# Optimization experiments

Measured on AMD Instinct MI355X. Metric: run time of the kernel, lower is better.

The kernel has to match this reference:

```python
import jax, jax.numpy as jnp
from jax import lax
import numpy as np

# --- config (torchvision Mask R-CNN RPN / RoIAlign defaults) ---
IMG = 800.0        # image size (square)
STRIDE = 4.0       # FPN level stride -> feature 200x200
K_PRE = 2000       # pre-NMS top-k proposals
K_POST = 512       # post-NMS proposals kept
IOU_THR = 0.7      # RPN NMS IoU threshold
OUT = 7            # RoIAlign output size
SR = 2             # RoIAlign sampling ratio
SCALE = 1.0 / STRIDE
BBOX_XFORM_CLIP = 4.135166556742356  # log(1000/16)


def setup_inputs() -> dict:
    key = jax.random.key(0)
    k1, k2, k3 = jax.random.split(key, 3)
    C, H, W = 256, 200, 200
    feature = jax.random.normal(k1, (C, H, W), jnp.float32)
    # anchor grid: 3 sizes per location, stride 4 (proper geometric anchors)
    sizes = np.array([32.0, 64.0, 128.0], np.float32)
    ys, xs = np.meshgrid(np.arange(H, dtype=np.float32) * STRIDE,
                         np.arange(W, dtype=np.float32) * STRIDE, indexing='ij')
    ctr = np.stack([xs, ys], axis=-1).reshape(-1, 1, 2)            # [HW,1,2] (x,y)
    half = np.stack([sizes / 2, sizes / 2], axis=-1)[None]          # [1,3,2]
    anchors = np.concatenate([ctr - half + 0 * half, ctr + half], axis=-1)
    anchors = np.broadcast_to(np.concatenate([ctr - half, ctr + half], -1),
                              (H * W, 3, 4)).reshape(-1, 4).astype(np.float32)
    N = anchors.shape[0]  # 120000
    objectness = jax.random.normal(k2, (N,), jnp.float32)
    deltas = jax.random.normal(k3, (N, 4), jnp.float32) * 0.1
    return {"feature": feature, "objectness": objectness,
            "deltas": deltas, "anchors": jnp.asarray(anchors)}


def decode_boxes(deltas, anchors):
    w = anchors[:, 2] - anchors[:, 0]
    h = anchors[:, 3] - anchors[:, 1]
    cx = anchors[:, 0] + 0.5 * w
    cy = anchors[:, 1] + 0.5 * h
    dx, dy = deltas[:, 0], deltas[:, 1]
    dw = jnp.minimum(deltas[:, 2], BBOX_XFORM_CLIP)
    dh = jnp.minimum(deltas[:, 3], BBOX_XFORM_CLIP)
    pcx = dx * w + cx
    pcy = dy * h + cy
    pw = jnp.exp(dw) * w
    ph = jnp.exp(dh) * h
    boxes = jnp.stack([pcx - 0.5 * pw, pcy - 0.5 * ph,
                       pcx + 0.5 * pw, pcy + 0.5 * ph], axis=-1)
    return jnp.clip(boxes, 0.0, IMG)


def pairwise_iou(b):  # b: [K,4]
    area = (b[:, 2] - b[:, 0]) * (b[:, 3] - b[:, 1])
    lt = jnp.maximum(b[:, None, :2], b[None, :, :2])
    rb = jnp.minimum(b[:, None, 2:], b[None, :, 2:])
    wh = jnp.maximum(rb - lt, 0.0)
    inter = wh[..., 0] * wh[..., 1]
    return inter / (area[:, None] + area[None, :] - inter + 1e-6)


def nms_suppress(boxes_sorted, iou_thr):
    # boxes sorted by descending score; returns keep mask [K]
    K = boxes_sorted.shape[0]
    iou = pairwise_iou(boxes_sorted)
    js = jnp.arange(K)
    def body(i, supp):
        row = (iou[i] > iou_thr) & (js > i)
        return jnp.where(supp[i], supp, supp | row)
    supp = lax.fori_loop(0, K, body, jnp.zeros((K,), bool))
    return ~supp


def roi_align(feature, boxes):
    # feature: [C,H,W]; boxes: [M,4] in image coords; aligned=False variant
    C, H, W = feature.shape
    P = OUT * SR
    def one(box):
        x1, y1, x2, y2 = box[0] * SCALE, box[1] * SCALE, box[2] * SCALE, box[3] * SCALE
        rw = jnp.maximum(x2 - x1, 1.0)
        rh = jnp.maximum(y2 - y1, 1.0)
        idx = jnp.arange(P, dtype=feature.dtype) + 0.5
        ys = y1 + idx * (rh / P)   # [P]
        xs = x1 + idx * (rw / P)
        yy, xx = jnp.meshgrid(ys, xs, indexing='ij')     # [P,P]
        y = jnp.clip(yy, 0.0, H - 1.0)
        x = jnp.clip(xx, 0.0, W - 1.0)
        y0 = jnp.floor(y).astype(jnp.int32)
        x0 = jnp.floor(x).astype(jnp.int32)
        y1i = jnp.minimum(y0 + 1, H - 1)
        x1i = jnp.minimum(x0 + 1, W - 1)
        ly = y - y0.astype(feature.dtype)
        lx = x - x0.astype(feature.dtype)
        v00 = feature[:, y0, x0]    # [C,P,P]
        v01 = feature[:, y0, x1i]
        v10 = feature[:, y1i, x0]
        v11 = feature[:, y1i, x1i]
        val = (v00 * (1 - ly) * (1 - lx) + v01 * (1 - ly) * lx
               + v10 * ly * (1 - lx) + v11 * ly * lx)  # [C,P,P]
        return val.reshape(C, OUT, SR, OUT, SR).mean(axis=(2, 4))  # [C,7,7]
    return jax.vmap(one)(boxes)


def reference(feature, objectness, deltas, anchors):
    boxes = decode_boxes(deltas, anchors)                    # [N,4]
    scores, idx = lax.top_k(objectness, K_PRE)               # pre-NMS top-k
    cand = boxes[idx]                                        # [K_PRE,4] sorted
    keep = nms_suppress(cand, IOU_THR)                       # [K_PRE] bool
    masked = jnp.where(keep, scores, -jnp.inf)
    _, fidx = lax.top_k(masked, K_POST)                      # post-NMS top-k
    final_boxes = cand[fidx]                                 # [K_POST,4]
    valid = keep[fidx].astype(feature.dtype)                 # [K_POST]
    roi = roi_align(feature, final_boxes)                    # [K_POST,256,7,7]
    return roi * valid[:, None, None, None]
```

## Files before the change

kernel.cpp:

```cpp
#include <hip/hip_runtime.h>
#include <cstdint>
#include <cstddef>

#define N_ANCH   120000
#define K_PRE    2000
#define K_POST   512
#define CAP      4096
#define NWORD    32
#define HBINS    4096
#define IOU_THR  0.7f
#define IMGF     800.0f
#define CLIPV    4.135166556742356f
#define FH       200
#define FW       200
#define FC       256
#define SCALE    0.25f

#define TROWS    96
#define NTILE    21
#define CH       8

#define CG       16
#define TPE      4

typedef unsigned long long u64;
typedef float f2u __attribute__((ext_vector_type(2), aligned(4)));

struct Ws {
    uint32_t T;
    uint32_t cnt;
    int32_t  nk;
    uint32_t pad;
    u64      combo[CAP];
    float4   cand[K_PRE];
    int      rows[K_POST];
    u64      mask[(size_t)K_PRE * NWORD];
};

__device__ inline uint32_t fkey(float f) {
    uint32_t u = __float_as_uint(f);
    return (u & 0x80000000u) ? ~u : (u | 0x80000000u);
}

__global__ __launch_bounds__(1024) void zero_k(Ws* __restrict__ ws) {
    uint32_t* h = (uint32_t*)ws->mask;
    for (int i = threadIdx.x; i < HBINS; i += 1024) h[i] = 0u;
    if (threadIdx.x == 0) { ws->cnt = 0u; ws->nk = 0; ws->T = 0u; }
}

__global__ __launch_bounds__(256) void hist_k(const float* __restrict__ obj,
                                              uint32_t* __restrict__ hist) {
    __shared__ uint32_t h[HBINS];
    for (int i = threadIdx.x; i < HBINS; i += 256) h[i] = 0u;
    __syncthreads();
    const float4* o4 = (const float4*)obj;
    for (int i = blockIdx.x * 256 + threadIdx.x; i < N_ANCH / 4; i += gridDim.x * 256) {
        float4 v = o4[i];
        atomicAdd(&h[fkey(v.x) >> 20], 1u);
        atomicAdd(&h[fkey(v.y) >> 20], 1u);
        atomicAdd(&h[fkey(v.z) >> 20], 1u);
        atomicAdd(&h[fkey(v.w) >> 20], 1u);
    }
    __syncthreads();
    for (int i = threadIdx.x; i < HBINS; i += 256)
        if (h[i]) atomicAdd(&hist[i], h[i]);
}

__global__ __launch_bounds__(256) void gather_k(const float* __restrict__ obj,
                                                const uint32_t* __restrict__ hist,
                                                Ws* __restrict__ ws) {
    __shared__ uint32_t wsum[4];
    __shared__ uint32_t sT;
    const int tid = threadIdx.x;
    const int lane = tid & 63, wave = tid >> 6;
    uint32_t c[16]; uint32_t s = 0;
#pragma unroll
    for (int k = 0; k < 16; ++k) { c[k] = hist[HBINS - 1 - (16 * tid + k)]; s += c[k]; }
    uint32_t incl = s;
    for (int off = 1; off < 64; off <<= 1) {
        uint32_t t = __shfl_up(incl, off);
        if (lane >= off) incl += t;
    }
    if (lane == 63) wsum[wave] = incl;
    __syncthreads();
    uint32_t wpre = 0;
    for (int w2 = 0; w2 < wave; ++w2) wpre += wsum[w2];
    uint32_t before = wpre + incl - s;
#pragma unroll
    for (int k = 0; k < 16; ++k) {
        uint32_t after = before + c[k];
        if (before < K_PRE && after >= K_PRE)
            sT = (uint32_t)(HBINS - 1 - (16 * tid + k)) << 20;
        before = after;
    }
    __syncthreads();
    const uint32_t T = sT;
    int i = blockIdx.x * 256 + tid;
    if (i >= N_ANCH / 4) return;
    float4 v = ((const float4*)obj)[i];
    float vals[4] = {v.x, v.y, v.z, v.w};
#pragma unroll
    for (int k = 0; k < 4; ++k) {
        uint32_t u = fkey(vals[k]);
        if (u >= T) {
            uint32_t pos = atomicAdd(&ws->cnt, 1u);
            if (pos < CAP)
                ws->combo[pos] = ((u64)(~u) << 32) | (uint32_t)(4 * i + k);
        }
    }
}

__global__ __launch_bounds__(256) void rank_decode_k(const float* __restrict__ deltas,
                                                     const float* __restrict__ anchors,
                                                     Ws* __restrict__ ws) {
    __shared__ u64 sc[CAP];
    const int tid = threadIdx.x;
    int M = (int)ws->cnt;
    if (M > CAP) M = CAP;
    const int ebase = blockIdx.x * (256 / TPE);
    if (ebase >= M) return;
    for (int e = tid; e < M; e += 256) sc[e] = ws->combo[e];
    __syncthreads();
    const int gid = ebase + tid / TPE;
    const int sub = tid & (TPE - 1);
    if (gid >= M) return;
    const u64 mine = sc[gid];
    int cnt = 0;
    int j = sub;
    for (; j + 3 * TPE < M; j += 4 * TPE) {
        u64 a = sc[j], b = sc[j + TPE], c = sc[j + 2 * TPE], d = sc[j + 3 * TPE];
        cnt += (int)(a < mine) + (int)(b < mine) + (int)(c < mine) + (int)(d < mine);
    }
    for (; j < M; j += TPE) cnt += (int)(sc[j] < mine);
    cnt += __shfl_xor(cnt, 1);
    cnt += __shfl_xor(cnt, 2);
    if (sub == 0 && cnt < K_PRE) {
        const uint32_t idx = (uint32_t)(mine & 0xFFFFFFFFull);
        float a0 = anchors[idx * 4 + 0], a1 = anchors[idx * 4 + 1];
        float a2 = anchors[idx * 4 + 2], a3 = anchors[idx * 4 + 3];
        float d0 = deltas[idx * 4 + 0],  d1 = deltas[idx * 4 + 1];
        float d2 = fminf(deltas[idx * 4 + 2], CLIPV);
        float d3 = fminf(deltas[idx * 4 + 3], CLIPV);
        float w = a2 - a0, h = a3 - a1;
        float cx = a0 + 0.5f * w, cy = a1 + 0.5f * h;
        float pcx = d0 * w + cx, pcy = d1 * h + cy;
        float pw = expf(d2) * w, ph = expf(d3) * h;
        float x1 = fminf(fmaxf(pcx - 0.5f * pw, 0.0f), IMGF);
        float y1 = fminf(fmaxf(pcy - 0.5f * ph, 0.0f), IMGF);
        float x2 = fminf(fmaxf(pcx + 0.5f * pw, 0.0f), IMGF);
        float y2 = fminf(fmaxf(pcy + 0.5f * ph, 0.0f), IMGF);
        ws->cand[cnt] = make_float4(x1, y1, x2, y2);
    }
}

__global__ __launch_bounds__(256) void nms_mask_k(Ws* __restrict__ ws) {
    const int i = blockIdx.x;
    const int lane = threadIdx.x & 63;
    const int wave = threadIdx.x >> 6;
    const float4 bi = ws->cand[i];
    const float ai = (bi.z - bi.x) * (bi.w - bi.y);
    for (int wd = wave; wd < NWORD; wd += 4) {
        int j = wd * 64 + lane;
        bool bit = false;
        if (j < K_PRE && j > i) {
            float4 bj = ws->cand[j];
            float aj = (bj.z - bj.x) * (bj.w - bj.y);
            float xx1 = fmaxf(bi.x, bj.x);
            float yy1 = fmaxf(bi.y, bj.y);
            float xx2 = fminf(bi.z, bj.z);
            float yy2 = fminf(bi.w, bj.w);
            float ww = fmaxf(xx2 - xx1, 0.0f);
            float hh = fmaxf(yy2 - yy1, 0.0f);
            float inter = ww * hh;
            float iou = inter / (ai + aj - inter + 1e-6f);
            bit = iou > IOU_THR;
        }
        u64 bal = __ballot(bit);
        if (lane == 0) ws->mask[(size_t)i * NWORD + wd] = bal;
    }
}

__global__ __launch_bounds__(512) void scan_roi_k(const float* __restrict__ feat,
                                                  Ws* __restrict__ ws,
                                                  float* __restrict__ out) {
    __shared__ __align__(16) u64 sbuf[2][TROWS * NWORD];
    __shared__ int s_stop;
    __shared__ int sRow;
    const int tid = threadIdx.x;
    const int lane = tid & 63;
    const int wave = tid >> 6;

    if (blockIdx.x == 0) {
        const int lmod = lane & 31;
        const u64* __restrict__ mask = ws->mask;
        {
            const ulonglong2* src = (const ulonglong2*)mask;
            ulonglong2* dst = (ulonglong2*)sbuf[0];
            for (int e = tid; e < TROWS * NWORD / 2; e += 512) dst[e] = src[e];
        }
        if (tid == 0) s_stop = 0;
        __syncthreads();

        u64 supp = 0ull;
        int pubtot = 0;
        const u64 valid = (lane < NWORD - 1) ? ~0ull
                        : (lane == NWORD - 1 ? ((1ull << (K_PRE - (NWORD - 1) * 64)) - 1ull)
                                             : 0ull);
        for (int t = 0; t < NTILE; ++t) {
            const int base = t * TROWS;
            const int nb = min(TROWS, K_PRE - base);
            if (wave == 0) {
                const u64* sm = sbuf[t & 1];
                u64 A[CH], B[CH];
#pragma unroll
                for (int b = 0; b < CH; ++b) A[b] = sm[b * NWORD + lmod];
                for (int s = 0; s < nb; s += 2 * CH) {
                    const bool hasB = (s + CH) < nb;
                    if (hasB) {
#pragma unroll
                        for (int b = 0; b < CH; ++b) B[b] = sm[(s + CH + b) * NWORD + lmod];
                    }
                    {
                        const int w = (base + s) >> 6;
                        const int bofs = (base + s) & 63;
                        u64 keptw = 0ull;
                        if (lane == w) {
                            u64 cur = supp;
#pragma unroll
                            for (int b = 0; b < CH; ++b) {
                                u64 bit = (cur >> (bofs + b)) & 1ull;
                                u64 sel = bit - 1ull;
                                cur |= A[b] & sel;
                                keptw |= sel & (1ull << b);
                            }
                            supp = cur;
                        }
                        u64 kb = __shfl(keptw, w);
#pragma unroll
                        for (int b = 0; b < CH; ++b) {
                            u64 sel = 0ull - ((kb >> b) & 1ull);
                            supp |= A[b] & sel;
                        }
                    }
                    if (hasB) {
                        if (s + 2 * CH < nb) {
#pragma unroll
                            for (int b = 0; b < CH; ++b)
                                A[b] = sm[(s + 2 * CH + b) * NWORD + lmod];
                        }
                        const int w = (base + s + CH) >> 6;
                        const int bofs = (base + s + CH) & 63;
                        u64 keptw = 0ull;
                        if (lane == w) {
                            u64 cur = supp;
#pragma unroll
                            for (int b = 0; b < CH; ++b) {
                                u64 bit = (cur >> (bofs + b)) & 1ull;
                                u64 sel = bit - 1ull;
                                cur |= B[b] & sel;
                                keptw |= sel & (1ull << b);
                            }
                            supp = cur;
                        }
                        u64 kb = __shfl(keptw, w);
#pragma unroll
                        for (int b = 0; b < CH; ++b) {
                            u64 sel = 0ull - ((kb >> b) & 1ull);
                            supp |= B[b] & sel;
                        }
                    }
                }
                {
                    const int w0 = lane << 6;
                    int lo = base - w0;      if (lo < 0)  lo = 0;
                    int hi = base + nb - w0; if (hi > 64) hi = 64;
                    u64 rmask = 0ull;
                    if (hi > lo) {
                        u64 mh = (hi >= 64) ? ~0ull : ((1ull << hi) - 1ull);
                        u64 ml = (lo <= 0) ? 0ull : ((1ull << lo) - 1ull);
                        rmask = mh & ~ml;
                    }
                    u64 keepn = (~supp) & valid & rmask;
                    int c = __popcll(keepn);
                    int incl = c;
                    for (int off = 1; off < 64; off <<= 1) {
                        int tt = __shfl_up(incl, off);
                        if (lane >= off) incl += tt;
                    }
                    int pos = pubtot + incl - c;
                    u64 kw = keepn;
                    while (kw) {
                        int b = __ffsll((unsigned long long)kw) - 1;
                        kw &= kw - 1ull;
                        if (pos < K_POST)
                            __hip_atomic_store(&ws->rows[pos], w0 + b,
                                               __ATOMIC_RELAXED, __HIP_MEMORY_SCOPE_AGENT);
                        ++pos;
                    }
                    pubtot += __shfl(incl, 63);
                    int pr = pubtot < K_POST ? pubtot : K_POST;
                    if (lane == 0) {
                        __hip_atomic_store(&ws->T, (uint32_t)pr,
                                           __ATOMIC_RELEASE, __HIP_MEMORY_SCOPE_AGENT);
                        if (pubtot >= K_POST) s_stop = 1;
                    }
                }
            } else if (t + 1 < NTILE) {
                const int nbase = (t + 1) * TROWS;
                const int npairs = (min(TROWS, K_PRE - nbase) * NWORD) / 2;
                const ulonglong2* src = (const ulonglong2*)(mask + (size_t)nbase * NWORD);
                ulonglong2* dst = (ulonglong2*)sbuf[(t + 1) & 1];
                for (int e = tid - 64; e < npairs; e += 448) dst[e] = src[e];
            }
            __syncthreads();
            if (s_stop) break;
        }

        if (wave == 0) {
            for (int rr = pubtot + lane; rr < K_POST; rr += 64)
                __hip_atomic_store(&ws->rows[rr], -1,
                                   __ATOMIC_RELAXED, __HIP_MEMORY_SCOPE_AGENT);
            if (lane == 0) {
                ws->nk = pubtot;
                __hip_atomic_store(&ws->T, (uint32_t)K_POST,
                                   __ATOMIC_RELEASE, __HIP_MEMORY_SCOPE_AGENT);
            }
        }
        return;
    }

    const int u = (int)blockIdx.x - 1;
    const int r = u >> 3;
    const int xcd = u & 7;
    const int h = tid >> 8;
    const int tid2 = tid & 255;
    const int cg = xcd + 8 * h;
    const int cbase = cg * CG;

    if (tid == 0) {
        while (__hip_atomic_load(&ws->T, __ATOMIC_RELAXED, __HIP_MEMORY_SCOPE_AGENT)
               <= (uint32_t)r)
            __builtin_amdgcn_s_sleep(16);
        (void)__hip_atomic_load(&ws->T, __ATOMIC_ACQUIRE, __HIP_MEMORY_SCOPE_AGENT);
        sRow = __hip_atomic_load(&ws->rows[r], __ATOMIC_RELAXED, __HIP_MEMORY_SCOPE_AGENT);
    }
    __syncthreads();
    const int row = sRow;
    float* oblk = out + (size_t)r * (FC * 49) + (size_t)cbase * 49;

    if (row < 0) {
        for (int e = tid2; e < CG * 49; e += 256) oblk[e] = 0.0f;
        return;
    }
    if (tid2 >= 245) return;

    const int p = tid2 % 49;
    const int cslot = tid2 / 49;
    const int oy = p / 7, ox = p % 7;

    const float4 bx = ws->cand[row];
    const float x1 = bx.x * SCALE, y1 = bx.y * SCALE;
    const float x2 = bx.z * SCALE, y2 = bx.w * SCALE;
    const float rw = fmaxf(x2 - x1, 1.0f);
    const float rh = fmaxf(y2 - y1, 1.0f);
    const float stepx = rw / 14.0f;
    const float stepy = rh / 14.0f;

    int    off0[4], off1[4];
    float4 w4[4];
#pragma unroll
    for (int sub = 0; sub < 4; ++sub) {
        const int sy = sub >> 1, sx = sub & 1;
        float yy = y1 + ((float)(2 * oy + sy) + 0.5f) * stepy;
        float y = fminf(fmaxf(yy, 0.0f), (float)(FH - 1));
        float fy0 = floorf(y);
        int iy0 = (int)fy0;
        int iy1 = min(iy0 + 1, FH - 1);
        float ly = y - fy0;
        float xx = x1 + ((float)(2 * ox + sx) + 0.5f) * stepx;
        float x = fminf(fmaxf(xx, 0.0f), (float)(FW - 1));
        float fx0 = floorf(x);
        int ix0 = (int)fx0;
        float lx = x - fx0;
        float wxl, wxr; int base;
        if (ix0 >= FW - 1) { base = FW - 2; wxl = 0.0f; wxr = 1.0f; }
        else               { base = ix0;    wxl = 1.0f - lx; wxr = lx; }
        float wy0 = 1.0f - ly, wy1 = ly;
        off0[sub] = iy0 * FW + base;
        off1[sub] = iy1 * FW + base;
        w4[sub] = make_float4(wy0 * wxl * 0.25f, wy0 * wxr * 0.25f,
                              wy1 * wxl * 0.25f, wy1 * wxr * 0.25f);
    }

    const float* fb = feat + (size_t)cbase * (FH * FW);
    const float* f0 = fb + (size_t)cslot * (FH * FW);
    const float* f1 = fb + (size_t)(cslot + 5) * (FH * FW);
    const float* f2 = fb + (size_t)(cslot + 10) * (FH * FW);
    f2u r0[8], r1[8], r2[8], r3[8];
#pragma unroll
    for (int sub = 0; sub < 4; ++sub) {
        r0[2 * sub]     = *(const f2u*)(f0 + off0[sub]);
        r0[2 * sub + 1] = *(const f2u*)(f0 + off1[sub]);
    }
#pragma unroll
    for (int sub = 0; sub < 4; ++sub) {
        r1[2 * sub]     = *(const f2u*)(f1 + off0[sub]);
        r1[2 * sub + 1] = *(const f2u*)(f1 + off1[sub]);
    }
#pragma unroll
    for (int sub = 0; sub < 4; ++sub) {
        r2[2 * sub]     = *(const f2u*)(f2 + off0[sub]);
        r2[2 * sub + 1] = *(const f2u*)(f2 + off1[sub]);
    }
    const bool has4 = (cslot == 0);
    if (has4) {
        const float* f3 = fb + (size_t)15 * (FH * FW);
#pragma unroll
        for (int sub = 0; sub < 4; ++sub) {
            r3[2 * sub]     = *(const f2u*)(f3 + off0[sub]);
            r3[2 * sub + 1] = *(const f2u*)(f3 + off1[sub]);
        }
    }

    float a0 = 0.0f, a1 = 0.0f, a2 = 0.0f;
#pragma unroll
    for (int sub = 0; sub < 4; ++sub) {
        a0 += w4[sub].x * r0[2 * sub].x + w4[sub].y * r0[2 * sub].y
            + w4[sub].z * r0[2 * sub + 1].x + w4[sub].w * r0[2 * sub + 1].y;
    }
#pragma unroll
    for (int sub = 0; sub < 4; ++sub) {
        a1 += w4[sub].x * r1[2 * sub].x + w4[sub].y * r1[2 * sub].y
            + w4[sub].z * r1[2 * sub + 1].x + w4[sub].w * r1[2 * sub + 1].y;
    }
#pragma unroll
    for (int sub = 0; sub < 4; ++sub) {
        a2 += w4[sub].x * r2[2 * sub].x + w4[sub].y * r2[2 * sub].y
            + w4[sub].z * r2[2 * sub + 1].x + w4[sub].w * r2[2 * sub + 1].y;
    }
    oblk[cslot * 49 + p] = a0;
    oblk[(cslot + 5) * 49 + p] = a1;
    oblk[(cslot + 10) * 49 + p] = a2;

    if (has4) {
        float a3 = 0.0f;
#pragma unroll
        for (int sub = 0; sub < 4; ++sub) {
            a3 += w4[sub].x * r3[2 * sub].x + w4[sub].y * r3[2 * sub].y
                + w4[sub].z * r3[2 * sub + 1].x + w4[sub].w * r3[2 * sub + 1].y;
        }
        oblk[15 * 49 + p] = a3;
    }
}

extern "C" void kernel_launch(void* const* d_in, const int* in_sizes, int n_in,
                              void* d_out, int out_size, void* d_ws, size_t ws_size,
                              hipStream_t stream) {
    const float* feature    = (const float*)d_in[0];
    const float* objectness = (const float*)d_in[1];
    const float* deltas     = (const float*)d_in[2];
    const float* anchors    = (const float*)d_in[3];
    Ws* ws = (Ws*)d_ws;
    uint32_t* hist = (uint32_t*)ws->mask;
    float* out = (float*)d_out;

    hipLaunchKernelGGL(zero_k, dim3(1), dim3(1024), 0, stream, ws);
    hipLaunchKernelGGL(hist_k, dim3(256), dim3(256), 0, stream, objectness, hist);
    hipLaunchKernelGGL(gather_k, dim3((N_ANCH / 4 + 255) / 256), dim3(256), 0, stream,
                       objectness, hist, ws);
    hipLaunchKernelGGL(rank_decode_k, dim3(CAP / (256 / TPE)), dim3(256), 0, stream,
                       deltas, anchors, ws);
    hipLaunchKernelGGL(nms_mask_k, dim3(K_PRE), dim3(256), 0, stream, ws);
    hipLaunchKernelGGL(scan_roi_k, dim3(1 + 8 * K_POST), dim3(512), 0, stream,
                       feature, ws, out);
}
```

Measured before the change: 200.8 us.

## Pair two RoIs per block and switch producer/consumer handoff to device atomics

Each RoIAlign block now covers two consecutive RoIs (one per 256-thread half) for a single channel group, where before it covered one RoI across two channel groups. This remaps the grid so blocks wait on a pair of rows. The NMS scan block raises its wave priority, and row publication uses atomicExch plus an explicit vmcnt wait instead of release/acquire atomics. Consumers poll with atomicAdd(0) and a bounded retry count. The goal is cheaper cross-block handoff and keeping the serial scan block from being starved by co-resident RoI blocks. The risks are weaker memory-ordering guarantees and a poll bound that could let a block read rows that are not yet ready.

```diff
diff --git a/kernel.cpp b/kernel.cpp
--- a/kernel.cpp
+++ b/kernel.cpp
@@ -185,12 +185,13 @@
                                                   float* __restrict__ out) {
     __shared__ __align__(16) u64 sbuf[2][TROWS * NWORD];
     __shared__ int s_stop;
-    __shared__ int sRow;
+    __shared__ int sRow[2];
     const int tid = threadIdx.x;
     const int lane = tid & 63;
     const int wave = tid >> 6;
 
     if (blockIdx.x == 0) {
+        __builtin_amdgcn_s_setprio(3);
         const int lmod = lane & 31;
         const u64* __restrict__ mask = ws->mask;
         {
@@ -293,15 +294,14 @@
                         int b = __ffsll((unsigned long long)kw) - 1;
                         kw &= kw - 1ull;
                         if (pos < K_POST)
-                            __hip_atomic_store(&ws->rows[pos], w0 + b,
-                                               __ATOMIC_RELAXED, __HIP_MEMORY_SCOPE_AGENT);
+                            atomicExch((int*)&ws->rows[pos], w0 + b);
                         ++pos;
                     }
                     pubtot += __shfl(incl, 63);
                     int pr = pubtot < K_POST ? pubtot : K_POST;
+                    asm volatile("s_waitcnt vmcnt(0)" ::: "memory");
                     if (lane == 0) {
-                        __hip_atomic_store(&ws->T, (uint32_t)pr,
-                                           __ATOMIC_RELEASE, __HIP_MEMORY_SCOPE_AGENT);
+                        atomicExch(&ws->T, (uint32_t)pr);
                         if (pubtot >= K_POST) s_stop = 1;
                     }
                 }
@@ -318,34 +318,35 @@
 
         if (wave == 0) {
             for (int rr = pubtot + lane; rr < K_POST; rr += 64)
-                __hip_atomic_store(&ws->rows[rr], -1,
-                                   __ATOMIC_RELAXED, __HIP_MEMORY_SCOPE_AGENT);
+                atomicExch((int*)&ws->rows[rr], -1);
+            asm volatile("s_waitcnt vmcnt(0)" ::: "memory");
             if (lane == 0) {
                 ws->nk = pubtot;
-                __hip_atomic_store(&ws->T, (uint32_t)K_POST,
-                                   __ATOMIC_RELEASE, __HIP_MEMORY_SCOPE_AGENT);
+                atomicExch(&ws->T, (uint32_t)K_POST);
             }
         }
         return;
     }
 
     const int u = (int)blockIdx.x - 1;
-    const int r = u >> 3;
-    const int xcd = u & 7;
+    const int q = (u >> 3) & 255;
+    const int cg = (u & 7) + 8 * (u >> 11);
     const int h = tid >> 8;
     const int tid2 = tid & 255;
-    const int cg = xcd + 8 * h;
+    const int r = 2 * q + h;
     const int cbase = cg * CG;
 
     if (tid == 0) {
-        while (__hip_atomic_load(&ws->T, __ATOMIC_RELAXED, __HIP_MEMORY_SCOPE_AGENT)
-               <= (uint32_t)r)
-            __builtin_amdgcn_s_sleep(16);
-        (void)__hip_atomic_load(&ws->T, __ATOMIC_ACQUIRE, __HIP_MEMORY_SCOPE_AGENT);
-        sRow = __hip_atomic_load(&ws->rows[r], __ATOMIC_RELAXED, __HIP_MEMORY_SCOPE_AGENT);
-    }
-    __syncthreads();
-    const int row = sRow;
+        int polls = 0;
+        while (atomicAdd(&ws->T, 0u) <= (uint32_t)(2 * q + 1) && polls < (1 << 20)) {
+            __builtin_amdgcn_s_sleep(32);
+            ++polls;
+        }
+        sRow[0] = atomicAdd((int*)&ws->rows[2 * q], 0);
+        sRow[1] = atomicAdd((int*)&ws->rows[2 * q + 1], 0);
+    }
+    __syncthreads();
+    const int row = sRow[h];
     float* oblk = out + (size_t)r * (FC * 49) + (size_t)cbase * 49;
 
     if (row < 0) {
@@ -471,6 +472,6 @@
     hipLaunchKernelGGL(rank_decode_k, dim3(CAP / (256 / TPE)), dim3(256), 0, stream,
                        deltas, anchors, ws);
     hipLaunchKernelGGL(nms_mask_k, dim3(K_PRE), dim3(256), 0, stream, ws);
-    hipLaunchKernelGGL(scan_roi_k, dim3(1 + 8 * K_POST), dim3(512), 0, stream,
+    hipLaunchKernelGGL(scan_roi_k, dim3(1 + 4096), dim3(512), 0, stream,
                        feature, ws, out);
 }
```

After: 208.5 us. 3.8% more time.
